# Kernel optimization log

Hardware: AMD Instinct MI355X
Metric: run time of the kernel (lower is better)

The kernel has to match this reference:

```python
import jax, jax.numpy as jnp
import numpy as np
from jax import lax

S = 48          # fixed crop size (original crops are ragged; fixed here for batching)
EPS = 0.1       # Sinkhorn entropic regularization
ITERS = 50      # Sinkhorn iterations
TINY = 1e-8


def setup_inputs() -> dict:
    key = jax.random.key(0)
    k1, k2, k3 = jax.random.split(key, 3)
    B, C, H, W = 16, 5, 160, 160
    hm_gt = jax.random.uniform(k1, (B, C, H, W), dtype=jnp.float32)
    hm_pred = jax.random.uniform(k2, (B, C, H, W), dtype=jnp.float32)
    tops = jax.random.randint(k3, (B, 8, 2), 0, 112, dtype=jnp.int32)  # (y, x) per rect
    return {"hm_gt": hm_gt, "hm_pred": hm_pred, "tops": tops}


def _geometry_distance(s):
    # pairwise Euclidean distance between pixel centers of an s x s crop -> [s*s, s*s]
    ys, xs = jnp.meshgrid(jnp.arange(s, dtype=jnp.float32),
                          jnp.arange(s, dtype=jnp.float32), indexing="ij")
    pts = jnp.stack([ys.ravel(), xs.ravel()], axis=-1)          # [s*s, 2]
    d2 = jnp.sum((pts[:, None, :] - pts[None, :, :]) ** 2, -1)  # [s*s, s*s]
    return jnp.sqrt(d2)


def _crop_all(hm, tops):
    # hm: [B, C, H, W], tops: [B, R, 2] -> crops [B, R, C, S, S]
    def crop_one(hm_b, top):  # hm_b [C,H,W], top [2]
        return lax.dynamic_slice(hm_b, (0, top[0], top[1]), (hm_b.shape[0], S, S))
    return jax.vmap(lambda hb, tb: jax.vmap(lambda t: crop_one(hb, t))(tb))(hm, tops)


def reference(hm_gt, hm_pred, tops):
    B, C, H, W = hm_gt.shape
    n = S * S
    dist = _geometry_distance(S)            # [n, n]
    K = jnp.exp(-dist / EPS)                # Gibbs kernel
    M = K * dist                            # for the transport cost readout

    a = _crop_all(hm_gt, tops).reshape(-1, n)    # [N, n]
    b = _crop_all(hm_pred, tops).reshape(-1, n)  # [N, n]
    a = a / (jnp.sum(a, -1, keepdims=True) + TINY)   # normalize to marginals
    b = b / (jnp.sum(b, -1, keepdims=True) + TINY)

    N = a.shape[0]
    u0 = jnp.full((N, n), 1.0 / n, dtype=a.dtype)
    v0 = jnp.full((N, n), 1.0 / n, dtype=a.dtype)

    def body(carry, _):
        u, v = carry
        v = b / (u @ K + TINY)      # [N,n] @ [n,n]
        u = a / (v @ K.T + TINY)
        return (u, v), None

    (u, v), _ = lax.scan(body, (u0, v0), None, length=ITERS)
    # loss per crop: sum_ij u_i K_ij dist_ij v_j
    loss = jnp.sum((u @ M) * v)
    return loss
```

## Files before the change

### kernel.cpp

```cpp
#include <hip/hip_runtime.h>

#define TINYF 1e-8f
#define NITER 50

__device__ __forceinline__ float bperm(int addr4, float v) {
    return __int_as_float(__builtin_amdgcn_ds_bpermute(addr4, __float_as_int(v)));
}
__device__ __forceinline__ float dpp_shr1(float v) {
    return __int_as_float(__builtin_amdgcn_update_dpp(0, __float_as_int(v), 0x111, 0xf, 0xf, true));
}
__device__ __forceinline__ float dpp_shl1(float v) {
    return __int_as_float(__builtin_amdgcn_update_dpp(0, __float_as_int(v), 0x101, 0xf, 0xf, true));
}

#define PREPF(C0_, C1_, C2_) \
    L2 = dpp_shr1(C1_); L1 = dpp_shr1(C2_); R1 = dpp_shl1(C0_); R2 = dpp_shl1(C1_); \
    s1a = L1 + C1_; s1b = C0_ + C2_; s1c = C1_ + R1; \
    s2a = L2 + C2_; s2b = L1 + R1; s2c = C0_ + R2;
#define PREPS(C0_, C1_, C2_) \
    L1 = dpp_shr1(C2_); R1 = dpp_shl1(C0_); \
    s1a = L1 + C1_; s1b = C0_ + C2_; s1c = C1_ + R1;
#define AT0(I, C0_, C1_, C2_, KA, KB, KC) \
    acc[I][0] += KA * C0_ + KB * s1a + KC * s2a; \
    acc[I][1] += KA * C1_ + KB * s1b + KC * s2b; \
    acc[I][2] += KA * C2_ + KB * s1c + KC * s2c;
#define AT0I(I, C0_, C1_, C2_, KA, KB, KC) \
    acc[I][0] = KA * C0_ + KB * s1a + KC * s2a; \
    acc[I][1] = KA * C1_ + KB * s1b + KC * s2b; \
    acc[I][2] = KA * C2_ + KB * s1c + KC * s2c;
#define AT1(I, C0_, C1_, C2_, KA, KB) \
    acc[I][0] += KA * C0_ + KB * s1a; \
    acc[I][1] += KA * C1_ + KB * s1b; \
    acc[I][2] += KA * C2_ + KB * s1c;
#define AT1I(I, C0_, C1_, C2_, KA, KB) \
    acc[I][0] = KA * C0_ + KB * s1a; \
    acc[I][1] = KA * C1_ + KB * s1b; \
    acc[I][2] = KA * C2_ + KB * s1c;
#define AT2(I, C0_, C1_, C2_, KA) \
    acc[I][0] += KA * C0_; \
    acc[I][1] += KA * C1_; \
    acc[I][2] += KA * C2_;
#define AT2I(I, C0_, C1_, C2_, KA) \
    acc[I][0] = KA * C0_; \
    acc[I][1] = KA * C1_; \
    acc[I][2] = KA * C2_;

__global__ void __launch_bounds__(256)
sinkhorn_4w(const float* __restrict__ hm_gt,
            const float* __restrict__ hm_pred,
            const int* __restrict__ tops,
            float* __restrict__ out) {
    __shared__ __align__(16) float EX[2][4][4][64];
    __shared__ float sred[2][4];

    const int t = threadIdx.x;
    const int W = t >> 6;
    const int l = t & 63;
    const int b = l >> 4, c = l & 15;
    const bool btop = (b == 0), bbot = (b == 3);
    const bool wtop = (W == 0), wbot = (W == 3);
    const int upA = ((l - 16) & 63) << 2;
    const int dnA = ((l + 16) & 63) << 2;

    const int blk = blockIdx.x;
    const int bi = blk / 40, rr = (blk / 5) % 8, cc = blk % 5;
    const int y0 = tops[(bi * 8 + rr) * 2 + 0];
    const int x0 = tops[(bi * 8 + rr) * 2 + 1];
    const float* srcA = hm_gt + (size_t)(bi * 5 + cc) * 25600;
    const float* srcB = hm_pred + (size_t)(bi * 5 + cc) * 25600;

    float va[3][3], vb[3][3];
    float sA = 0.f, sB = 0.f;
    const int rbase = y0 + 12 * W + 3 * b;
#pragma unroll
    for (int i = 0; i < 3; ++i) {
        const int g = (rbase + i) * 160 + x0 + 3 * c;
#pragma unroll
        for (int j = 0; j < 3; ++j) {
            const float A = srcA[g + j];
            const float B = srcB[g + j];
            va[i][j] = A; vb[i][j] = B;
            sA += A; sB += B;
        }
    }
#pragma unroll
    for (int o = 1; o < 64; o <<= 1) {
        sA += __shfl_xor(sA, o, 64);
        sB += __shfl_xor(sB, o, 64);
    }
    if (l == 0) { sred[0][W] = sA; sred[1][W] = sB; }
    __syncthreads();
    sA = sred[0][0] + sred[0][1] + sred[0][2] + sred[0][3];
    sB = sred[1][0] + sred[1][1] + sred[1][2] + sred[1][3];
    const float nA = 1.0f / (sA + TINYF);
    const float nB = 1.0f / (sB + TINYF);
#pragma unroll
    for (int i = 0; i < 3; ++i)
#pragma unroll
        for (int j = 0; j < 3; ++j) { va[i][j] *= nA; vb[i][j] *= nB; }

    const float e10 = expf(-1.0f / 0.1f);
    const float e2  = expf(-sqrtf(2.0f) / 0.1f);
    const float e20 = expf(-2.0f / 0.1f);

    float xu[3][3], xv[3][3], acc[3][3];
    const float u0 = 1.0f / 2304.0f;
#pragma unroll
    for (int i = 0; i < 3; ++i)
#pragma unroll
        for (int j = 0; j < 3; ++j) xu[i][j] = u0;

    auto publish = [&](const float (&y)[3][3], int p) {
        if (btop) {
            *(float4*)&EX[p][W][0][c * 4] = make_float4(y[0][0], y[0][1], y[0][2], 0.f);
            *(float4*)&EX[p][W][1][c * 4] = make_float4(y[1][0], y[1][1], y[1][2], 0.f);
        }
        if (bbot) {
            *(float4*)&EX[p][W][2][c * 4] = make_float4(y[1][0], y[1][1], y[1][2], 0.f);
            *(float4*)&EX[p][W][3][c * 4] = make_float4(y[2][0], y[2][1], y[2][2], 0.f);
        }
        __syncthreads();
    };

    auto conv = [&](const float (&x)[3][3], int p,
                    float K00, float K01, float K02,
                    float K10, float K11, float K20) {
        float qA[3] = {0.f, 0.f, 0.f}, qB[3] = {0.f, 0.f, 0.f};
        float qC[3] = {0.f, 0.f, 0.f}, qD[3] = {0.f, 0.f, 0.f};
        if (btop && !wtop) {
            float4 f0 = *(const float4*)&EX[p][W - 1][2][c * 4];
            float4 f1 = *(const float4*)&EX[p][W - 1][3][c * 4];
            qA[0] = f0.x; qA[1] = f0.y; qA[2] = f0.z;
            qB[0] = f1.x; qB[1] = f1.y; qB[2] = f1.z;
        }
        if (bbot && !wbot) {
            float4 f0 = *(const float4*)&EX[p][W + 1][0][c * 4];
            float4 f1 = *(const float4*)&EX[p][W + 1][1][c * 4];
            qC[0] = f0.x; qC[1] = f0.y; qC[2] = f0.z;
            qD[0] = f1.x; qD[1] = f1.y; qD[2] = f1.z;
        }
        float tA[3], tB[3], tC[3], tD[3];
#pragma unroll
        for (int j = 0; j < 3; ++j) {
            tA[j] = bperm(upA, x[1][j]);
            tB[j] = bperm(upA, x[2][j]);
            tC[j] = bperm(dnA, x[0][j]);
            tD[j] = bperm(dnA, x[1][j]);
        }

        float L1, L2, R1, R2, s1a, s1b, s1c, s2a, s2b, s2c;
        PREPF(x[0][0], x[0][1], x[0][2])
        AT0I(0, x[0][0], x[0][1], x[0][2], K00, K01, K02)
        AT1I(1, x[0][0], x[0][1], x[0][2], K10, K11)
        AT2I(2, x[0][0], x[0][1], x[0][2], K20)
        PREPF(x[1][0], x[1][1], x[1][2])
        AT1(0, x[1][0], x[1][1], x[1][2], K10, K11)
        AT0(1, x[1][0], x[1][1], x[1][2], K00, K01, K02)
        AT1(2, x[1][0], x[1][1], x[1][2], K10, K11)
        PREPF(x[2][0], x[2][1], x[2][2])
        AT2(0, x[2][0], x[2][1], x[2][2], K20)
        AT1(1, x[2][0], x[2][1], x[2][2], K10, K11)
        AT0(2, x[2][0], x[2][1], x[2][2], K00, K01, K02)

        float hA[3], hB[3], hC[3], hD[3];
#pragma unroll
        for (int j = 0; j < 3; ++j) {
            hA[j] = btop ? qA[j] : tA[j];
            hB[j] = btop ? qB[j] : tB[j];
            hC[j] = bbot ? qC[j] : tC[j];
            hD[j] = bbot ? qD[j] : tD[j];
        }
        PREPS(hB[0], hB[1], hB[2])
        AT1(0, hB[0], hB[1], hB[2], K10, K11)
        AT2(1, hB[0], hB[1], hB[2], K20)
        AT2(0, hA[0], hA[1], hA[2], K20)
        PREPS(hC[0], hC[1], hC[2])
        AT2(1, hC[0], hC[1], hC[2], K20)
        AT1(2, hC[0], hC[1], hC[2], K10, K11)
        AT2(2, hD[0], hD[1], hD[2], K20)
    };

    publish(xu, 0);

#pragma unroll 1
    for (int it = 0; it < NITER; ++it) {
        conv(xu, 0, 1.0f, e10, e20, e10, e2, e20);
#pragma unroll
        for (int i = 0; i < 3; ++i)
#pragma unroll
            for (int j = 0; j < 3; ++j)
                xv[i][j] = vb[i][j] * __builtin_amdgcn_rcpf(acc[i][j] + TINYF);
        publish(xv, 1);

        conv(xv, 1, 1.0f, e10, e20, e10, e2, e20);
#pragma unroll
        for (int i = 0; i < 3; ++i)
#pragma unroll
            for (int j = 0; j < 3; ++j)
                xu[i][j] = va[i][j] * __builtin_amdgcn_rcpf(acc[i][j] + TINYF);
        publish(xu, 0);
    }

    const float s2f = sqrtf(2.0f);
    const float m01 = e10, m02 = e20 * 2.0f, m11 = e2 * s2f;
    conv(xu, 0, 0.0f, m01, m02, m01, m11, m02);
    float lsum = 0.f;
#pragma unroll
    for (int i = 0; i < 3; ++i)
#pragma unroll
        for (int j = 0; j < 3; ++j)
            lsum += acc[i][j] * xv[i][j];

#pragma unroll
    for (int o = 1; o < 64; o <<= 1) lsum += __shfl_xor(lsum, o, 64);
    if (l == 0) sred[0][W] = lsum;
    __syncthreads();
    if (t == 0)
        atomicAdd(out, sred[0][0] + sred[0][1] + sred[0][2] + sred[0][3]);
}

extern "C" void kernel_launch(void* const* d_in, const int* in_sizes, int n_in,
                              void* d_out, int out_size, void* d_ws, size_t ws_size,
                              hipStream_t stream) {
    (void)in_sizes; (void)n_in; (void)out_size; (void)d_ws; (void)ws_size;
    const float* hm_gt = (const float*)d_in[0];
    const float* hm_pred = (const float*)d_in[1];
    const int* tops = (const int*)d_in[2];
    float* out = (float*)d_out;

    hipMemsetAsync(out, 0, sizeof(float), stream);
    sinkhorn_4w<<<dim3(640), dim3(256), 0, stream>>>(hm_gt, hm_pred, tops, out);
}
```

Measured before the change: 198.4 us.

## Pack two crops per block into float2 for packed FP32 math

Each block now processes two Sinkhorn problems, storing all per-pixel state as two-wide float vectors so the stencil arithmetic can map to packed FP32 instructions. The shared-memory halo buffer is widened to hold both crops, and the grid is halved with a launch-bounds occupancy hint. This aims to cut VALU instruction count and amortize barriers and lane shuffles across two problems. The cost is doubled register pressure and fewer blocks, which lowers parallelism across CUs.

```diff
diff --git a/kernel.cpp b/kernel.cpp
--- a/kernel.cpp
+++ b/kernel.cpp
@@ -3,14 +3,28 @@
 #define TINYF 1e-8f
 #define NITER 50
 
-__device__ __forceinline__ float bperm(int addr4, float v) {
-    return __int_as_float(__builtin_amdgcn_ds_bpermute(addr4, __float_as_int(v)));
-}
-__device__ __forceinline__ float dpp_shr1(float v) {
+typedef __attribute__((ext_vector_type(2))) float v2f;
+
+__device__ __forceinline__ float dpp_shr1_s(float v) {
     return __int_as_float(__builtin_amdgcn_update_dpp(0, __float_as_int(v), 0x111, 0xf, 0xf, true));
 }
-__device__ __forceinline__ float dpp_shl1(float v) {
+__device__ __forceinline__ float dpp_shl1_s(float v) {
     return __int_as_float(__builtin_amdgcn_update_dpp(0, __float_as_int(v), 0x101, 0xf, 0xf, true));
+}
+__device__ __forceinline__ v2f dpp_shr1(v2f v) {
+    v2f r; r.x = dpp_shr1_s(v.x); r.y = dpp_shr1_s(v.y); return r;
+}
+__device__ __forceinline__ v2f dpp_shl1(v2f v) {
+    v2f r; r.x = dpp_shl1_s(v.x); r.y = dpp_shl1_s(v.y); return r;
+}
+__device__ __forceinline__ v2f bperm2(int addr4, v2f v) {
+    v2f r;
+    r.x = __int_as_float(__builtin_amdgcn_ds_bpermute(addr4, __float_as_int(v.x)));
+    r.y = __int_as_float(__builtin_amdgcn_ds_bpermute(addr4, __float_as_int(v.y)));
+    return r;
+}
+__device__ __forceinline__ v2f rcp2(v2f v) {
+    v2f r; r.x = __builtin_amdgcn_rcpf(v.x); r.y = __builtin_amdgcn_rcpf(v.y); return r;
 }
 
 #define PREPF(C0_, C1_, C2_) \
@@ -45,13 +59,14 @@
     acc[I][1] = KA * C1_; \
     acc[I][2] = KA * C2_;
 
-__global__ void __launch_bounds__(256)
-sinkhorn_4w(const float* __restrict__ hm_gt,
+__global__ void __launch_bounds__(256, 2)
+sinkhorn_pk(const float* __restrict__ hm_gt,
             const float* __restrict__ hm_pred,
             const int* __restrict__ tops,
             float* __restrict__ out) {
-    __shared__ __align__(16) float EX[2][4][4][64];
-    __shared__ float sred[2][4];
+    __shared__ __align__(16) float EXP[2][4][4][96];
+    __shared__ v2f sredA[4], sredB[4];
+    __shared__ float slw[4];
 
     const int t = threadIdx.x;
     const int W = t >> 6;
@@ -62,38 +77,48 @@
     const int upA = ((l - 16) & 63) << 2;
     const int dnA = ((l + 16) & 63) << 2;
 
-    const int blk = blockIdx.x;
-    const int bi = blk / 40, rr = (blk / 5) % 8, cc = blk % 5;
-    const int y0 = tops[(bi * 8 + rr) * 2 + 0];
-    const int x0 = tops[(bi * 8 + rr) * 2 + 1];
-    const float* srcA = hm_gt + (size_t)(bi * 5 + cc) * 25600;
-    const float* srcB = hm_pred + (size_t)(bi * 5 + cc) * 25600;
-
-    float va[3][3], vb[3][3];
-    float sA = 0.f, sB = 0.f;
-    const int rbase = y0 + 12 * W + 3 * b;
+    const int g = blockIdx.x;
+    const int k0 = 2 * g, k1 = 2 * g + 1;
+    const int bi0 = k0 / 40, rr0 = (k0 / 5) % 8, cc0 = k0 % 5;
+    const int bi1 = k1 / 40, rr1 = (k1 / 5) % 8, cc1 = k1 % 5;
+    const int y00 = tops[(bi0 * 8 + rr0) * 2 + 0];
+    const int x00 = tops[(bi0 * 8 + rr0) * 2 + 1];
+    const int y01 = tops[(bi1 * 8 + rr1) * 2 + 0];
+    const int x01 = tops[(bi1 * 8 + rr1) * 2 + 1];
+    const float* gt0 = hm_gt   + (size_t)(bi0 * 5 + cc0) * 25600;
+    const float* pr0 = hm_pred + (size_t)(bi0 * 5 + cc0) * 25600;
+    const float* gt1 = hm_gt   + (size_t)(bi1 * 5 + cc1) * 25600;
+    const float* pr1 = hm_pred + (size_t)(bi1 * 5 + cc1) * 25600;
+
+    v2f va[3][3], vb[3][3];
+    v2f sA = {0.f, 0.f}, sB = {0.f, 0.f};
+    const int rb0 = y00 + 12 * W + 3 * b;
+    const int rb1 = y01 + 12 * W + 3 * b;
 #pragma unroll
     for (int i = 0; i < 3; ++i) {
-        const int g = (rbase + i) * 160 + x0 + 3 * c;
+        const int g0 = (rb0 + i) * 160 + x00 + 3 * c;
+        const int g1 = (rb1 + i) * 160 + x01 + 3 * c;
 #pragma unroll
         for (int j = 0; j < 3; ++j) {
-            const float A = srcA[g + j];
-            const float B = srcB[g + j];
+            v2f A, B;
+            A.x = gt0[g0 + j]; A.y = gt1[g1 + j];
+            B.x = pr0[g0 + j]; B.y = pr1[g1 + j];
             va[i][j] = A; vb[i][j] = B;
             sA += A; sB += B;
         }
     }
 #pragma unroll
     for (int o = 1; o < 64; o <<= 1) {
-        sA += __shfl_xor(sA, o, 64);
-        sB += __shfl_xor(sB, o, 64);
+        sA.x += __shfl_xor(sA.x, o, 64); sA.y += __shfl_xor(sA.y, o, 64);
+        sB.x += __shfl_xor(sB.x, o, 64); sB.y += __shfl_xor(sB.y, o, 64);
     }
-    if (l == 0) { sred[0][W] = sA; sred[1][W] = sB; }
+    if (l == 0) { sredA[W] = sA; sredB[W] = sB; }
     __syncthreads();
-    sA = sred[0][0] + sred[0][1] + sred[0][2] + sred[0][3];
-    sB = sred[1][0] + sred[1][1] + sred[1][2] + sred[1][3];
-    const float nA = 1.0f / (sA + TINYF);
-    const float nB = 1.0f / (sB + TINYF);
+    sA = sredA[0] + sredA[1] + sredA[2] + sredA[3];
+    sB = sredB[0] + sredB[1] + sredB[2] + sredB[3];
+    v2f nA, nB;
+    nA.x = 1.0f / (sA.x + TINYF); nA.y = 1.0f / (sA.y + TINYF);
+    nB.x = 1.0f / (sB.x + TINYF); nB.y = 1.0f / (sB.y + TINYF);
 #pragma unroll
     for (int i = 0; i < 3; ++i)
 #pragma unroll
@@ -103,52 +128,51 @@
     const float e2  = expf(-sqrtf(2.0f) / 0.1f);
     const float e20 = expf(-2.0f / 0.1f);
 
-    float xu[3][3], xv[3][3], acc[3][3];
+    v2f xu[3][3], xv[3][3], acc[3][3];
     const float u0 = 1.0f / 2304.0f;
 #pragma unroll
     for (int i = 0; i < 3; ++i)
 #pragma unroll
-        for (int j = 0; j < 3; ++j) xu[i][j] = u0;
-
-    auto publish = [&](const float (&y)[3][3], int p) {
+        for (int j = 0; j < 3; ++j) { xu[i][j].x = u0; xu[i][j].y = u0; }
+
+    auto publish = [&](const v2f (&y)[3][3], int p) {
         if (btop) {
-            *(float4*)&EX[p][W][0][c * 4] = make_float4(y[0][0], y[0][1], y[0][2], 0.f);
-            *(float4*)&EX[p][W][1][c * 4] = make_float4(y[1][0], y[1][1], y[1][2], 0.f);
+            *(float4*)&EXP[p][W][0][c * 4] = make_float4(y[0][0].x, y[0][0].y, y[0][1].x, y[0][1].y);
+            *(v2f*)&EXP[p][W][0][64 + c * 2] = y[0][2];
+            *(float4*)&EXP[p][W][1][c * 4] = make_float4(y[1][0].x, y[1][0].y, y[1][1].x, y[1][1].y);
+            *(v2f*)&EXP[p][W][1][64 + c * 2] = y[1][2];
         }
         if (bbot) {
-            *(float4*)&EX[p][W][2][c * 4] = make_float4(y[1][0], y[1][1], y[1][2], 0.f);
-            *(float4*)&EX[p][W][3][c * 4] = make_float4(y[2][0], y[2][1], y[2][2], 0.f);
+            *(float4*)&EXP[p][W][2][c * 4] = make_float4(y[1][0].x, y[1][0].y, y[1][1].x, y[1][1].y);
+            *(v2f*)&EXP[p][W][2][64 + c * 2] = y[1][2];
+            *(float4*)&EXP[p][W][3][c * 4] = make_float4(y[2][0].x, y[2][0].y, y[2][1].x, y[2][1].y);
+            *(v2f*)&EXP[p][W][3][64 + c * 2] = y[2][2];
         }
         __syncthreads();
     };
 
-    auto conv = [&](const float (&x)[3][3], int p,
+    auto readrow = [&](int p, int w, int slot, v2f (&q)[3]) {
+        const float4 f = *(const float4*)&EXP[p][w][slot][c * 4];
+        q[0].x = f.x; q[0].y = f.y; q[1].x = f.z; q[1].y = f.w;
+        q[2] = *(const v2f*)&EXP[p][w][slot][64 + c * 2];
+    };
+
+    auto conv = [&](const v2f (&x)[3][3], int p,
                     float K00, float K01, float K02,
                     float K10, float K11, float K20) {
-        float qA[3] = {0.f, 0.f, 0.f}, qB[3] = {0.f, 0.f, 0.f};
-        float qC[3] = {0.f, 0.f, 0.f}, qD[3] = {0.f, 0.f, 0.f};
-        if (btop && !wtop) {
-            float4 f0 = *(const float4*)&EX[p][W - 1][2][c * 4];
-            float4 f1 = *(const float4*)&EX[p][W - 1][3][c * 4];
-            qA[0] = f0.x; qA[1] = f0.y; qA[2] = f0.z;
-            qB[0] = f1.x; qB[1] = f1.y; qB[2] = f1.z;
-        }
-        if (bbot && !wbot) {
-            float4 f0 = *(const float4*)&EX[p][W + 1][0][c * 4];
-            float4 f1 = *(const float4*)&EX[p][W + 1][1][c * 4];
-            qC[0] = f0.x; qC[1] = f0.y; qC[2] = f0.z;
-            qD[0] = f1.x; qD[1] = f1.y; qD[2] = f1.z;
-        }
-        float tA[3], tB[3], tC[3], tD[3];
+        v2f qA[3] = {}, qB[3] = {}, qC[3] = {}, qD[3] = {};
+        if (btop && !wtop) { readrow(p, W - 1, 2, qA); readrow(p, W - 1, 3, qB); }
+        if (bbot && !wbot) { readrow(p, W + 1, 0, qC); readrow(p, W + 1, 1, qD); }
+        v2f tA[3], tB[3], tC[3], tD[3];
 #pragma unroll
         for (int j = 0; j < 3; ++j) {
-            tA[j] = bperm(upA, x[1][j]);
-            tB[j] = bperm(upA, x[2][j]);
-            tC[j] = bperm(dnA, x[0][j]);
-            tD[j] = bperm(dnA, x[1][j]);
-        }
-
-        float L1, L2, R1, R2, s1a, s1b, s1c, s2a, s2b, s2c;
+            tA[j] = bperm2(upA, x[1][j]);
+            tB[j] = bperm2(upA, x[2][j]);
+            tC[j] = bperm2(dnA, x[0][j]);
+            tD[j] = bperm2(dnA, x[1][j]);
+        }
+
+        v2f L1, L2, R1, R2, s1a, s1b, s1c, s2a, s2b, s2c;
         PREPF(x[0][0], x[0][1], x[0][2])
         AT0I(0, x[0][0], x[0][1], x[0][2], K00, K01, K02)
         AT1I(1, x[0][0], x[0][1], x[0][2], K10, K11)
@@ -162,7 +186,7 @@
         AT1(1, x[2][0], x[2][1], x[2][2], K10, K11)
         AT0(2, x[2][0], x[2][1], x[2][2], K00, K01, K02)
 
-        float hA[3], hB[3], hC[3], hD[3];
+        v2f hA[3], hB[3], hC[3], hD[3];
 #pragma unroll
         for (int j = 0; j < 3; ++j) {
             hA[j] = btop ? qA[j] : tA[j];
@@ -189,7 +213,7 @@
         for (int i = 0; i < 3; ++i)
 #pragma unroll
             for (int j = 0; j < 3; ++j)
-                xv[i][j] = vb[i][j] * __builtin_amdgcn_rcpf(acc[i][j] + TINYF);
+                xv[i][j] = vb[i][j] * rcp2(acc[i][j] + TINYF);
         publish(xv, 1);
 
         conv(xv, 1, 1.0f, e10, e20, e10, e2, e20);
@@ -197,26 +221,27 @@
         for (int i = 0; i < 3; ++i)
 #pragma unroll
             for (int j = 0; j < 3; ++j)
-                xu[i][j] = va[i][j] * __builtin_amdgcn_rcpf(acc[i][j] + TINYF);
+                xu[i][j] = va[i][j] * rcp2(acc[i][j] + TINYF);
         publish(xu, 0);
     }
 
     const float s2f = sqrtf(2.0f);
     const float m01 = e10, m02 = e20 * 2.0f, m11 = e2 * s2f;
     conv(xu, 0, 0.0f, m01, m02, m01, m11, m02);
-    float lsum = 0.f;
+    v2f lsum2 = {0.f, 0.f};
 #pragma unroll
     for (int i = 0; i < 3; ++i)
 #pragma unroll
         for (int j = 0; j < 3; ++j)
-            lsum += acc[i][j] * xv[i][j];
+            lsum2 += acc[i][j] * xv[i][j];
+    float lsum = lsum2.x + lsum2.y;
 
 #pragma unroll
     for (int o = 1; o < 64; o <<= 1) lsum += __shfl_xor(lsum, o, 64);
-    if (l == 0) sred[0][W] = lsum;
+    if (l == 0) slw[W] = lsum;
     __syncthreads();
     if (t == 0)
-        atomicAdd(out, sred[0][0] + sred[0][1] + sred[0][2] + sred[0][3]);
+        atomicAdd(out, slw[0] + slw[1] + slw[2] + slw[3]);
 }
 
 extern "C" void kernel_launch(void* const* d_in, const int* in_sizes, int n_in,
@@ -229,5 +254,5 @@
     float* out = (float*)d_out;
 
     hipMemsetAsync(out, 0, sizeof(float), stream);
-    sinkhorn_4w<<<dim3(640), dim3(256), 0, stream>>>(hm_gt, hm_pred, tops, out);
-}
+    sinkhorn_pk<<<dim3(320), dim3(256), 0, stream>>>(hm_gt, hm_pred, tops, out);
+}
```

Measured after the change: 213.5 us. 7.6% more time.
